# Optimization experiments

Measured on AMD Instinct MI355X. Metric: run time of the kernel, lower is better.

Reference implementation:

```python
import jax, jax.numpy as jnp
import numpy as np

BETA = 0.01  # soft-threshold level (init kwarg)
EPS = 1e-12


def vector_to_toeplitz(v):
    # v: [2N-1] complex generator; T[i, j] = v[N-1 + i - j], shape [N, N]
    n = (v.shape[0] + 1) // 2
    ii = jnp.arange(n)[:, None]
    jj = jnp.arange(n)[None, :]
    return v[(n - 1) + ii - jj]


def soft_thresh(z, beta):
    # complex soft-threshold (proximal op of beta*||.||_1):
    # z * max(|z| - beta, 0) / |z|
    mag = jnp.abs(z)
    scale = jnp.maximum(mag - beta, 0.0) / jnp.maximum(mag, EPS)
    return z * scale.astype(z.real.dtype)


def setup_inputs() -> dict:
    key = jax.random.key(0)
    ks = jax.random.split(key, 8)
    N, M, B = 1024, 256, 1024
    d = jnp.float32
    return {
        "v_re": jax.random.normal(ks[0], (2 * N - 1,), d),
        "v_im": jax.random.normal(ks[1], (2 * N - 1,), d),
        "W2_re": jax.random.normal(ks[2], (N, M), d) / np.sqrt(M),
        "W2_im": jax.random.normal(ks[3], (N, M), d) / np.sqrt(M),
        "x_re": jax.random.normal(ks[4], (N, B), d),
        "x_im": jax.random.normal(ks[5], (N, B), d),
        "y_re": jax.random.normal(ks[6], (M, B), d),
        "y_im": jax.random.normal(ks[7], (M, B), d),
    }


def reference(v_re, v_im, W2_re, W2_im, x_re, x_im, y_re, y_im):
    v = jax.lax.complex(v_re, v_im)      # [2N-1]
    W2 = jax.lax.complex(W2_re, W2_im)   # [N, M] (= A^H)
    x = jax.lax.complex(x_re, x_im)      # [N, B]
    y = jax.lax.complex(y_re, y_im)      # [M, B]
    W1 = vector_to_toeplitz(v)           # [N, N] Toeplitz
    # tpm(W1, x) + W2 @ y, then complex soft-threshold
    z = soft_thresh(W1 @ x + W2 @ y, BETA)  # [N, B]
    return z
```

## Files before the change

kernel.cpp:

```cpp
#include <hip/hip_runtime.h>
#include <hip/hip_fp16.h>
#include <cstdint>
#include <cstddef>


#define K_DIM 2560
#define BETA_F 0.01f
#define EPS_F  1e-12f

typedef __attribute__((ext_vector_type(8))) _Float16 half8;
typedef __attribute__((ext_vector_type(4))) _Float16 half4;
typedef __attribute__((ext_vector_type(4))) float   floatx4;

__device__ alignas(16) _Float16 g_Ap[1024 * K_DIM];
__device__ alignas(16) _Float16 g_Bt[2048 * K_DIM];

__global__ __launch_bounds__(256) void build_all(
    const float* __restrict__ v_re, const float* __restrict__ v_im,
    const float* __restrict__ W2_re, const float* __restrict__ W2_im,
    const float* __restrict__ x_re, const float* __restrict__ x_im,
    const float* __restrict__ y_re, const float* __restrict__ y_im)
{
    const int bx = blockIdx.x;
    if (bx < 1280) {
        int t = bx * 256 + threadIdx.x;
        int i  = t / 320;
        int c  = t - i * 320;
        int kp = c * 8;
        half8 h;
        if (kp < 1024) {
#pragma unroll
            for (int j = 0; j < 8; ++j) h[j] = (_Float16)v_re[1023 + i - kp - j];
        } else if (kp < 1280) {
            const float* s = W2_re + i * 256 + (kp - 1024);
#pragma unroll
            for (int j = 0; j < 8; ++j) h[j] = (_Float16)s[j];
        } else if (kp < 2304) {
            int k2 = kp - 1280;
#pragma unroll
            for (int j = 0; j < 8; ++j) h[j] = (_Float16)v_im[1023 + i - k2 - j];
        } else {
            const float* s = W2_im + i * 256 + (kp - 2304);
#pragma unroll
            for (int j = 0; j < 8; ++j) h[j] = (_Float16)s[j];
        }
        *reinterpret_cast<half8*>(g_Ap + (size_t)i * K_DIM + kp) = h;
        return;
    }
    __shared__ float lre[32][33];
    __shared__ float lim[32][33];
    int idx = bx - 1280;
    int bk  = idx % 40;
    int by  = idx / 40;
    const float* sre = (bk < 32) ? x_re : y_re;
    const float* sim = (bk < 32) ? x_im : y_im;
    int kb   = (bk < 32) ? bk : (bk - 32);
    int koff = (bk < 32) ? 0 : 1024;
    int k0 = kb * 32;
    int n0 = by * 32;
    int tid = threadIdx.x;
    int tx = tid & 31, ty = tid >> 5;
#pragma unroll
    for (int s = 0; s < 4; ++s) {
        int kk = ty + 8 * s;
        lre[kk][tx] = sre[(size_t)(k0 + kk) * 1024 + n0 + tx];
        lim[kk][tx] = sim[(size_t)(k0 + kk) * 1024 + n0 + tx];
    }
    __syncthreads();
    int lane_n = tid >> 3;
    int kq     = (tid & 7) * 4;
    half4 hre, him, hmim;
#pragma unroll
    for (int j = 0; j < 4; ++j) {
        float re = lre[kq + j][lane_n];
        float im = lim[kq + j][lane_n];
        hre[j]  = (_Float16)re;
        him[j]  = (_Float16)im;
        hmim[j] = (_Float16)(-im);
    }
    int n = n0 + lane_n;
    size_t kk2 = (size_t)koff + k0 + kq;
    _Float16* r0 = g_Bt + (size_t)(2 * n)     * K_DIM;
    _Float16* r1 = g_Bt + (size_t)(2 * n + 1) * K_DIM;
    *reinterpret_cast<half4*>(r0 + kk2)        = hre;
    *reinterpret_cast<half4*>(r0 + kk2 + 1280) = hmim;
    *reinterpret_cast<half4*>(r1 + kk2)        = him;
    *reinterpret_cast<half4*>(r1 + kk2 + 1280) = hre;
}

__device__ __forceinline__ void load_lds16(const void* g, void* l) {
    __builtin_amdgcn_global_load_lds(
        (const __attribute__((address_space(1))) void*)g,
        (__attribute__((address_space(3))) void*)l, 16, 0, 0);
}

__global__ __launch_bounds__(256, 4) void gemm_fused(float* __restrict__ out,
                                                     int out_n)
{
    __shared__ __align__(16) _Float16 As[2 * 2 * 64 * 32];
    __shared__ __align__(16) _Float16 Bs[2 * 2 * 64 * 32];

    const int tid  = threadIdx.x;
    const int lane = tid & 63;
    const int w    = tid >> 6;
    const int wm   = w >> 1;
    const int wn   = w & 1;

    const int bid = blockIdx.x;
    const int xcd = bid & 7;
    const int t   = bid >> 3;
    const int mi0 = ((xcd & 1) * 8 + (t & 7)) * 64;
    const int ni0 = ((xcd >> 1) * 8 + (t >> 3)) * 64;

    floatx4 acc[2][2];
#pragma unroll
    for (int a = 0; a < 2; ++a)
#pragma unroll
        for (int b = 0; b < 2; ++b) acc[a][b] = (floatx4)0.0f;

    const int rowS  = (w * 16) + (lane >> 2);
    const int chunk = (lane & 3) ^ ((lane >> 3) & 3);
    const _Float16* gAl = g_Ap + (size_t)(mi0 + rowS) * K_DIM + chunk * 8;
    const _Float16* gBl = g_Bt + (size_t)(ni0 + rowS) * K_DIM + chunk * 8;
    char* asBase = (char*)As + w * 1024;
    char* bsBase = (char*)Bs + w * 1024;

    const int rowA = lane & 15;
    const int q    = lane >> 4;
    const int coff = (q ^ ((rowA >> 1) & 3)) * 16;

    const int NIT = K_DIM / 64;

#pragma unroll
    for (int ks = 0; ks < 2; ++ks) {
        load_lds16(gAl + ks * 32, asBase + ks * 4096);
        load_lds16(gBl + ks * 32, bsBase + ks * 4096);
    }
    __syncthreads();

    for (int kt = 0; kt < NIT; ++kt) {
        const int cur = kt & 1;
        const int nxt = cur ^ 1;
        if (kt + 1 < NIT) {
            const _Float16* ga = gAl + (size_t)(kt + 1) * 64;
            const _Float16* gb = gBl + (size_t)(kt + 1) * 64;
#pragma unroll
            for (int ks = 0; ks < 2; ++ks) {
                load_lds16(ga + ks * 32, asBase + nxt * 8192 + ks * 4096);
                load_lds16(gb + ks * 32, bsBase + nxt * 8192 + ks * 4096);
            }
        }
        const char* Ab = (const char*)As + cur * 8192;
        const char* Bb = (const char*)Bs + cur * 8192;
        half8 af[2][2], bf[2][2];
#pragma unroll
        for (int mi = 0; mi < 2; ++mi) {
            int r = wm * 32 + mi * 16 + rowA;
            af[mi][0] = *reinterpret_cast<const half8*>(Ab + r * 64 + coff);
            af[mi][1] = *reinterpret_cast<const half8*>(Ab + 4096 + r * 64 + coff);
        }
#pragma unroll
        for (int ni = 0; ni < 2; ++ni) {
            int r = wn * 32 + ni * 16 + rowA;
            bf[ni][0] = *reinterpret_cast<const half8*>(Bb + r * 64 + coff);
            bf[ni][1] = *reinterpret_cast<const half8*>(Bb + 4096 + r * 64 + coff);
        }
#pragma unroll
        for (int mi = 0; mi < 2; ++mi)
#pragma unroll
            for (int ni = 0; ni < 2; ++ni) {
                acc[mi][ni] = __builtin_amdgcn_mfma_f32_16x16x32_f16(
                    af[mi][0], bf[ni][0], acc[mi][ni], 0, 0, 0);
                acc[mi][ni] = __builtin_amdgcn_mfma_f32_16x16x32_f16(
                    af[mi][1], bf[ni][1], acc[mi][ni], 0, 0, 0);
            }
        __syncthreads();
    }

    const int colL  = lane & 15;
    const int rquad = (lane >> 4) * 4;
#pragma unroll
    for (int mi = 0; mi < 2; ++mi)
#pragma unroll
        for (int ni = 0; ni < 2; ++ni)
#pragma unroll
            for (int r = 0; r < 4; ++r) {
                float c = acc[mi][ni][r];
                float p = __shfl_xor(c, 1, 64);
                float mag = sqrtf(c * c + p * p);
                float s = fmaxf(mag - BETA_F, 0.0f) / fmaxf(mag, EPS_F);
                int row = mi0 + wm * 32 + mi * 16 + rquad + r;
                int col = ni0 + wn * 32 + ni * 16 + colL;
                if ((col & 1) == 0) {
                    size_t idx = (size_t)row * 1024 + (col >> 1);
                    if (idx < (size_t)out_n) out[idx] = c * s;
                }
            }
}

extern "C" void kernel_launch(void* const* d_in, const int* in_sizes, int n_in,
                              void* d_out, int out_size, void* d_ws, size_t ws_size,
                              hipStream_t stream) {
    (void)d_ws; (void)ws_size; (void)in_sizes; (void)n_in;
    const float* v_re  = (const float*)d_in[0];
    const float* v_im  = (const float*)d_in[1];
    const float* W2_re = (const float*)d_in[2];
    const float* W2_im = (const float*)d_in[3];
    const float* x_re  = (const float*)d_in[4];
    const float* x_im  = (const float*)d_in[5];
    const float* y_re  = (const float*)d_in[6];
    const float* y_im  = (const float*)d_in[7];
    float* out = (float*)d_out;

    build_all<<<2560, 256, 0, stream>>>(v_re, v_im, W2_re, W2_im,
                                        x_re, x_im, y_re, y_im);
    gemm_fused<<<512, 256, 0, stream>>>(out, out_size);
}
```

Baseline: 115.8 us.

## Replace direct-to-LDS loads with register-staged prefetch and deeper K tile

```diff
diff --git a/kernel.cpp b/kernel.cpp
--- a/kernel.cpp
+++ b/kernel.cpp
@@ -88,17 +88,11 @@
     *reinterpret_cast<half4*>(r1 + kk2 + 1280) = hre;
 }
 
-__device__ __forceinline__ void load_lds16(const void* g, void* l) {
-    __builtin_amdgcn_global_load_lds(
-        (const __attribute__((address_space(1))) void*)g,
-        (__attribute__((address_space(3))) void*)l, 16, 0, 0);
-}
-
-__global__ __launch_bounds__(256, 4) void gemm_fused(float* __restrict__ out,
+__global__ __launch_bounds__(256, 2) void gemm_fused(float* __restrict__ out,
                                                      int out_n)
 {
-    __shared__ __align__(16) _Float16 As[2 * 2 * 64 * 32];
-    __shared__ __align__(16) _Float16 Bs[2 * 2 * 64 * 32];
+    __shared__ __align__(16) _Float16 As[2 * 4 * 64 * 32];
+    __shared__ __align__(16) _Float16 Bs[2 * 4 * 64 * 32];
 
     const int tid  = threadIdx.x;
     const int lane = tid & 63;
@@ -118,62 +112,86 @@
 #pragma unroll
         for (int b = 0; b < 2; ++b) acc[a][b] = (floatx4)0.0f;
 
-    const int rowS  = (w * 16) + (lane >> 2);
-    const int chunk = (lane & 3) ^ ((lane >> 3) & 3);
-    const _Float16* gAl = g_Ap + (size_t)(mi0 + rowS) * K_DIM + chunk * 8;
-    const _Float16* gBl = g_Bt + (size_t)(ni0 + rowS) * K_DIM + chunk * 8;
-    char* asBase = (char*)As + w * 1024;
-    char* bsBase = (char*)Bs + w * 1024;
+    const int rS = tid >> 2;
+    const int jS = tid & 3;
+    const int s0 = ((rS & 15) >> 1) & 3;
+    char* asW = (char*)As + rS * 64 + ((jS ^ s0) * 16);
+    char* bsW = (char*)Bs + rS * 64 + ((jS ^ s0) * 16);
+    const _Float16* gA = g_Ap + (size_t)(mi0 + rS) * K_DIM + jS * 8;
+    const _Float16* gB = g_Bt + (size_t)(ni0 + rS) * K_DIM + jS * 8;
 
     const int rowA = lane & 15;
     const int q    = lane >> 4;
     const int coff = (q ^ ((rowA >> 1) & 3)) * 16;
 
-    const int NIT = K_DIM / 64;
-
-#pragma unroll
-    for (int ks = 0; ks < 2; ++ks) {
-        load_lds16(gAl + ks * 32, asBase + ks * 4096);
-        load_lds16(gBl + ks * 32, bsBase + ks * 4096);
+    const int NIT = K_DIM / 128;
+
+    half8 sA[2][4], sB[2][4];
+
+    {
+        half8 tA[4], tB[4];
+#pragma unroll
+        for (int ks = 0; ks < 4; ++ks) {
+            tA[ks] = *reinterpret_cast<const half8*>(gA + ks * 32);
+            tB[ks] = *reinterpret_cast<const half8*>(gB + ks * 32);
+        }
+#pragma unroll
+        for (int ks = 0; ks < 4; ++ks) {
+            sA[1][ks] = *reinterpret_cast<const half8*>(gA + 128 + ks * 32);
+            sB[1][ks] = *reinterpret_cast<const half8*>(gB + 128 + ks * 32);
+        }
+#pragma unroll
+        for (int ks = 0; ks < 4; ++ks) {
+            *reinterpret_cast<half8*>(asW + ks * 4096) = tA[ks];
+            *reinterpret_cast<half8*>(bsW + ks * 4096) = tB[ks];
+        }
     }
     __syncthreads();
 
+#pragma unroll 2
     for (int kt = 0; kt < NIT; ++kt) {
         const int cur = kt & 1;
         const int nxt = cur ^ 1;
+        if (kt + 2 < NIT) {
+            const _Float16* ga = gA + (size_t)(kt + 2) * 128;
+            const _Float16* gb = gB + (size_t)(kt + 2) * 128;
+#pragma unroll
+            for (int ks = 0; ks < 4; ++ks) {
+                sA[cur][ks] = *reinterpret_cast<const half8*>(ga + ks * 32);
+                sB[cur][ks] = *reinterpret_cast<const half8*>(gb + ks * 32);
+            }
+        }
+        const char* Ab = (const char*)As + cur * 16384;
+        const char* Bb = (const char*)Bs + cur * 16384;
+#pragma unroll
+        for (int ks = 0; ks < 4; ++ks) {
+            half8 af[2], bf[2];
+#pragma unroll
+            for (int mi = 0; mi < 2; ++mi) {
+                int r = wm * 32 + mi * 16 + rowA;
+                af[mi] = *reinterpret_cast<const half8*>(Ab + ks * 4096 + r * 64 + coff);
+            }
+#pragma unroll
+            for (int ni = 0; ni < 2; ++ni) {
+                int r = wn * 32 + ni * 16 + rowA;
+                bf[ni] = *reinterpret_cast<const half8*>(Bb + ks * 4096 + r * 64 + coff);
+            }
+#pragma unroll
+            for (int mi = 0; mi < 2; ++mi)
+#pragma unroll
+                for (int ni = 0; ni < 2; ++ni)
+                    acc[mi][ni] = __builtin_amdgcn_mfma_f32_16x16x32_f16(
+                        af[mi], bf[ni], acc[mi][ni], 0, 0, 0);
+        }
         if (kt + 1 < NIT) {
-            const _Float16* ga = gAl + (size_t)(kt + 1) * 64;
-            const _Float16* gb = gBl + (size_t)(kt + 1) * 64;
-#pragma unroll
-            for (int ks = 0; ks < 2; ++ks) {
-                load_lds16(ga + ks * 32, asBase + nxt * 8192 + ks * 4096);
-                load_lds16(gb + ks * 32, bsBase + nxt * 8192 + ks * 4096);
-            }
-        }
-        const char* Ab = (const char*)As + cur * 8192;
-        const char* Bb = (const char*)Bs + cur * 8192;
-        half8 af[2][2], bf[2][2];
-#pragma unroll
-        for (int mi = 0; mi < 2; ++mi) {
-            int r = wm * 32 + mi * 16 + rowA;
-            af[mi][0] = *reinterpret_cast<const half8*>(Ab + r * 64 + coff);
-            af[mi][1] = *reinterpret_cast<const half8*>(Ab + 4096 + r * 64 + coff);
-        }
-#pragma unroll
-        for (int ni = 0; ni < 2; ++ni) {
-            int r = wn * 32 + ni * 16 + rowA;
-            bf[ni][0] = *reinterpret_cast<const half8*>(Bb + r * 64 + coff);
-            bf[ni][1] = *reinterpret_cast<const half8*>(Bb + 4096 + r * 64 + coff);
-        }
-#pragma unroll
-        for (int mi = 0; mi < 2; ++mi)
-#pragma unroll
-            for (int ni = 0; ni < 2; ++ni) {
-                acc[mi][ni] = __builtin_amdgcn_mfma_f32_16x16x32_f16(
-                    af[mi][0], bf[ni][0], acc[mi][ni], 0, 0, 0);
-                acc[mi][ni] = __builtin_amdgcn_mfma_f32_16x16x32_f16(
-                    af[mi][1], bf[ni][1], acc[mi][ni], 0, 0, 0);
-            }
+            char* aw = asW + nxt * 16384;
+            char* bw = bsW + nxt * 16384;
+#pragma unroll
+            for (int ks = 0; ks < 4; ++ks) {
+                *reinterpret_cast<half8*>(aw + ks * 4096) = sA[nxt][ks];
+                *reinterpret_cast<half8*>(bw + ks * 4096) = sB[nxt][ks];
+            }
+        }
         __syncthreads();
     }
 
```

Result: faster. 107.3 us, median of 2 (-7.4%).

## Load GEMM fragments directly from global memory with register prefetch ring

Applied to the files above, without the earlier changes.

```diff
diff --git a/kernel.cpp b/kernel.cpp
--- a/kernel.cpp
+++ b/kernel.cpp
@@ -88,18 +88,9 @@
     *reinterpret_cast<half4*>(r1 + kk2 + 1280) = hre;
 }
 
-__device__ __forceinline__ void load_lds16(const void* g, void* l) {
-    __builtin_amdgcn_global_load_lds(
-        (const __attribute__((address_space(1))) void*)g,
-        (__attribute__((address_space(3))) void*)l, 16, 0, 0);
-}
-
 __global__ __launch_bounds__(256, 4) void gemm_fused(float* __restrict__ out,
                                                      int out_n)
 {
-    __shared__ __align__(16) _Float16 As[2 * 2 * 64 * 32];
-    __shared__ __align__(16) _Float16 Bs[2 * 2 * 64 * 32];
-
     const int tid  = threadIdx.x;
     const int lane = tid & 63;
     const int w    = tid >> 6;
@@ -112,69 +103,54 @@
     const int mi0 = ((xcd & 1) * 8 + (t & 7)) * 64;
     const int ni0 = ((xcd >> 1) * 8 + (t >> 3)) * 64;
 
+    const int rowA = lane & 15;
+    const int q8   = (lane >> 4) * 8;
+
+    const _Float16* aP[2];
+    const _Float16* bP[2];
+#pragma unroll
+    for (int mi = 0; mi < 2; ++mi)
+        aP[mi] = g_Ap + (size_t)(mi0 + wm * 32 + mi * 16 + rowA) * K_DIM + q8;
+#pragma unroll
+    for (int ni = 0; ni < 2; ++ni)
+        bP[ni] = g_Bt + (size_t)(ni0 + wn * 32 + ni * 16 + rowA) * K_DIM + q8;
+
     floatx4 acc[2][2];
 #pragma unroll
     for (int a = 0; a < 2; ++a)
 #pragma unroll
         for (int b = 0; b < 2; ++b) acc[a][b] = (floatx4)0.0f;
 
-    const int rowS  = (w * 16) + (lane >> 2);
-    const int chunk = (lane & 3) ^ ((lane >> 3) & 3);
-    const _Float16* gAl = g_Ap + (size_t)(mi0 + rowS) * K_DIM + chunk * 8;
-    const _Float16* gBl = g_Bt + (size_t)(ni0 + rowS) * K_DIM + chunk * 8;
-    char* asBase = (char*)As + w * 1024;
-    char* bsBase = (char*)Bs + w * 1024;
+    const int NKS = K_DIM / 32;
 
-    const int rowA = lane & 15;
-    const int q    = lane >> 4;
-    const int coff = (q ^ ((rowA >> 1) & 3)) * 16;
+    half8 pa[4][2], pb[4][2];
+#pragma unroll
+    for (int s = 0; s < 4; ++s) {
+#pragma unroll
+        for (int mi = 0; mi < 2; ++mi)
+            pa[s][mi] = *reinterpret_cast<const half8*>(aP[mi] + s * 32);
+#pragma unroll
+        for (int ni = 0; ni < 2; ++ni)
+            pb[s][ni] = *reinterpret_cast<const half8*>(bP[ni] + s * 32);
+    }
 
-    const int NIT = K_DIM / 64;
-
-#pragma unroll
-    for (int ks = 0; ks < 2; ++ks) {
-        load_lds16(gAl + ks * 32, asBase + ks * 4096);
-        load_lds16(gBl + ks * 32, bsBase + ks * 4096);
-    }
-    __syncthreads();
-
-    for (int kt = 0; kt < NIT; ++kt) {
-        const int cur = kt & 1;
-        const int nxt = cur ^ 1;
-        if (kt + 1 < NIT) {
-            const _Float16* ga = gAl + (size_t)(kt + 1) * 64;
-            const _Float16* gb = gBl + (size_t)(kt + 1) * 64;
-#pragma unroll
-            for (int ks = 0; ks < 2; ++ks) {
-                load_lds16(ga + ks * 32, asBase + nxt * 8192 + ks * 4096);
-                load_lds16(gb + ks * 32, bsBase + nxt * 8192 + ks * 4096);
-            }
-        }
-        const char* Ab = (const char*)As + cur * 8192;
-        const char* Bb = (const char*)Bs + cur * 8192;
-        half8 af[2][2], bf[2][2];
-#pragma unroll
-        for (int mi = 0; mi < 2; ++mi) {
-            int r = wm * 32 + mi * 16 + rowA;
-            af[mi][0] = *reinterpret_cast<const half8*>(Ab + r * 64 + coff);
-            af[mi][1] = *reinterpret_cast<const half8*>(Ab + 4096 + r * 64 + coff);
-        }
-#pragma unroll
-        for (int ni = 0; ni < 2; ++ni) {
-            int r = wn * 32 + ni * 16 + rowA;
-            bf[ni][0] = *reinterpret_cast<const half8*>(Bb + r * 64 + coff);
-            bf[ni][1] = *reinterpret_cast<const half8*>(Bb + 4096 + r * 64 + coff);
-        }
+#pragma unroll 4
+    for (int s = 0; s < NKS; ++s) {
+        const int slot = s & 3;
 #pragma unroll
         for (int mi = 0; mi < 2; ++mi)
 #pragma unroll
-            for (int ni = 0; ni < 2; ++ni) {
+            for (int ni = 0; ni < 2; ++ni)
                 acc[mi][ni] = __builtin_amdgcn_mfma_f32_16x16x32_f16(
-                    af[mi][0], bf[ni][0], acc[mi][ni], 0, 0, 0);
-                acc[mi][ni] = __builtin_amdgcn_mfma_f32_16x16x32_f16(
-                    af[mi][1], bf[ni][1], acc[mi][ni], 0, 0, 0);
-            }
-        __syncthreads();
+                    pa[slot][mi], pb[slot][ni], acc[mi][ni], 0, 0, 0);
+        if (s + 4 < NKS) {
+#pragma unroll
+            for (int mi = 0; mi < 2; ++mi)
+                pa[slot][mi] = *reinterpret_cast<const half8*>(aP[mi] + (s + 4) * 32);
+#pragma unroll
+            for (int ni = 0; ni < 2; ++ni)
+                pb[slot][ni] = *reinterpret_cast<const half8*>(bP[ni] + (s + 4) * 32);
+        }
     }
 
     const int colL  = lane & 15;
@@ -188,12 +164,12 @@
                 float c = acc[mi][ni][r];
                 float p = __shfl_xor(c, 1, 64);
                 float mag = sqrtf(c * c + p * p);
-                float s = fmaxf(mag - BETA_F, 0.0f) / fmaxf(mag, EPS_F);
+                float sc = fmaxf(mag - BETA_F, 0.0f) / fmaxf(mag, EPS_F);
                 int row = mi0 + wm * 32 + mi * 16 + rquad + r;
                 int col = ni0 + wn * 32 + ni * 16 + colL;
                 if ((col & 1) == 0) {
                     size_t idx = (size_t)row * 1024 + (col >> 1);
-                    if (idx < (size_t)out_n) out[idx] = c * s;
+                    if (idx < (size_t)out_n) out[idx] = c * sc;
                 }
             }
 }
```

After: 158.5 us. 1.37x slower.
